# Kernel tuning notes

Measured on AMD Instinct MI355X. Metric: run time of the kernel, lower is better.

## Reference

```python
import jax, jax.numpy as jnp
import numpy as np

NEG_INF = jnp.float32(-1e30)


def setup_inputs() -> dict:
    key = jax.random.key(0)
    ks = jax.random.split(key, 7)
    B, Lx, Lm, d = 4, 256, 256, 256
    return {
        "x": jax.random.normal(ks[0], (B, Lx, d), dtype=jnp.float32),
        "memory": jax.random.normal(ks[1], (B, Lm, d), dtype=jnp.float32),
        "memory_mask": jax.random.randint(ks[2], (B, Lm), 0, 2, dtype=jnp.int32),
        "ws1_w": jax.random.normal(ks[3], (d, d), dtype=jnp.float32) * 0.05,
        "ws1_b": jax.random.normal(ks[4], (d,), dtype=jnp.float32) * 0.05,
        "ws2_w": jax.random.normal(ks[5], (d, d), dtype=jnp.float32) * 0.05,
        "wst_w": jax.random.normal(ks[6], (1, d), dtype=jnp.float32) * 0.05,
    }


def reference(x, memory, memory_mask, ws1_w, ws1_b, ws2_w, wst_w):
    # x: [B, Lx, d], memory: [B, Lm, d]; torch Linear: y = x @ W.T + b
    item1 = jnp.einsum('bxd,ed->bxe', x, ws1_w) + ws1_b          # [B, Lx, d]
    item2 = jnp.einsum('bmd,ed->bme', memory, ws2_w)             # [B, Lm, d]
    item = jnp.tanh(item1[:, :, None, :] + item2[:, None, :, :])  # [B, Lx, Lm, d]
    S = jnp.einsum('bxmd,d->bxm', item, wst_w[0])                # [B, Lx, Lm]
    # agg_2_h uses the UNMASKED scores, softmax over Lx after transpose
    agg_2_h = jnp.einsum('bmx,bxd->bmd', jax.nn.softmax(S.transpose(0, 2, 1), axis=-1), x)
    # mask applied to S before the main attention readout
    S = jnp.where(memory_mask[:, None, :] == 0, NEG_INF, S)      # [B, Lx, Lm]
    out = jnp.einsum('bxm,bmd->bxd', jax.nn.softmax(S, axis=-1), memory)
    return (out, S, agg_2_h)
```

## Files before the change

kernel.cpp:

```cpp
#include <hip/hip_runtime.h>

static constexpr int NB = 4;
static constexpr int L  = 256;
static constexpr int D  = 256;

__device__ __forceinline__ float fast_rcp(float x) {
#if __has_builtin(__builtin_amdgcn_rcpf)
    return __builtin_amdgcn_rcpf(x);
#else
    return 1.0f / x;
#endif
}

__device__ __forceinline__ float fast_exp(float x) {
#if __has_builtin(__builtin_amdgcn_exp2f)
    return __builtin_amdgcn_exp2f(x * 1.4426950408889634f);
#else
    return __expf(x);
#endif
}

__device__ __forceinline__ float tanh_fast(float y) {
#if __has_builtin(__builtin_amdgcn_exp2f)
    float e = __builtin_amdgcn_exp2f(y * 2.8853900817779268f);
#else
    float e = __expf(2.0f * y);
#endif
    return fmaf(-2.0f, fast_rcp(e + 1.0f), 1.0f);
}

__global__ __launch_bounds__(256) void linear_kernel(
    const float* __restrict__ x, const float* __restrict__ mem,
    const float* __restrict__ w1, const float* __restrict__ b1,
    const float* __restrict__ w2,
    float* __restrict__ i1, float* __restrict__ i2)
{
    const int bid = blockIdx.x;
    const int rb  = (bid >> 3) * 32;
    const int cb  = (bid & 7) * 32;
    const int which = rb >= 1024;
    const int rloc  = which ? rb - 1024 : rb;
    const float* src = which ? mem : x;
    const float* W   = which ? w2  : w1;
    float*       dst = which ? i2  : i1;

    constexpr int P4 = 65;
    __shared__ __align__(16) float4 xs4[32 * P4];
    __shared__ __align__(16) float4 ws4[32 * P4];

    const int t = threadIdx.x;
    const float4* src4 = reinterpret_cast<const float4*>(src) + rloc * 64;
    const float4* Wg4  = reinterpret_cast<const float4*>(W)   + cb   * 64;
#pragma unroll
    for (int k = 0; k < 8; ++k) {
        int idx = k * 256 + t;
        int r = idx >> 6, c = idx & 63;
        xs4[r * P4 + c] = src4[r * 64 + c];
        ws4[r * P4 + c] = Wg4[r * 64 + c];
    }
    __syncthreads();

    const int rr = t >> 4, cc = t & 15;
    const float4* a0p = xs4 + rr * P4;
    const float4* a1p = xs4 + (rr + 16) * P4;
    const float4* w0p = ws4 + cc * P4;
    const float4* w1p = ws4 + (cc + 16) * P4;
    float acc00 = 0.f, acc01 = 0.f, acc10 = 0.f, acc11 = 0.f;
#pragma unroll 4
    for (int d4 = 0; d4 < 64; ++d4) {
        float4 a0 = a0p[d4], a1 = a1p[d4];
        float4 w0 = w0p[d4], w1 = w1p[d4];
        acc00 = fmaf(a0.x, w0.x, acc00); acc00 = fmaf(a0.y, w0.y, acc00);
        acc00 = fmaf(a0.z, w0.z, acc00); acc00 = fmaf(a0.w, w0.w, acc00);
        acc01 = fmaf(a0.x, w1.x, acc01); acc01 = fmaf(a0.y, w1.y, acc01);
        acc01 = fmaf(a0.z, w1.z, acc01); acc01 = fmaf(a0.w, w1.w, acc01);
        acc10 = fmaf(a1.x, w0.x, acc10); acc10 = fmaf(a1.y, w0.y, acc10);
        acc10 = fmaf(a1.z, w0.z, acc10); acc10 = fmaf(a1.w, w0.w, acc10);
        acc11 = fmaf(a1.x, w1.x, acc11); acc11 = fmaf(a1.y, w1.y, acc11);
        acc11 = fmaf(a1.z, w1.z, acc11); acc11 = fmaf(a1.w, w1.w, acc11);
    }
    const float bias0 = which ? 0.f : b1[cb + cc];
    const float bias1 = which ? 0.f : b1[cb + cc + 16];
    dst[(rloc + rr)      * D + cb + cc]      = acc00 + bias0;
    dst[(rloc + rr)      * D + cb + cc + 16] = acc01 + bias1;
    dst[(rloc + rr + 16) * D + cb + cc]      = acc10 + bias0;
    dst[(rloc + rr + 16) * D + cb + cc + 16] = acc11 + bias1;
}

__global__ __launch_bounds__(256) void score_kernel(
    const float* __restrict__ i1, const float* __restrict__ i2,
    const float* __restrict__ wst, const int* __restrict__ mask,
    float* __restrict__ outS, float* __restrict__ ST)
{
    const int bid = blockIdx.x;
    const int b   = bid >> 8;
    const int xt  = ((bid >> 4) & 15) * 16;
    const int mt  = (bid & 15) * 16;
    const int t   = threadIdx.x;

    constexpr int PAD = 260;
    __shared__ __align__(16) float s1[16 * PAD];
    __shared__ __align__(16) float s2[16 * PAD];
    __shared__ float stile[16 * 17];

    const float4* i14 = reinterpret_cast<const float4*>(i1) + (b * L + xt) * (D / 4);
    const float4* i24 = reinterpret_cast<const float4*>(i2) + (b * L + mt) * (D / 4);
    float4* s14 = reinterpret_cast<float4*>(s1);
    float4* s24 = reinterpret_cast<float4*>(s2);
#pragma unroll
    for (int k = 0; k < 4; ++k) {
        int idx = k * 256 + t;
        int r = idx >> 6, c = idx & 63;
        s14[r * (PAD / 4) + c] = i14[r * (D / 4) + c];
        s24[r * (PAD / 4) + c] = i24[r * (D / 4) + c];
    }
    __syncthreads();

    const int xl = t >> 4, ml = t & 15;
    const float4* a4 = s14 + xl * (PAD / 4);
    const float4* b4 = s24 + ml * (PAD / 4);
    const float4* w4 = reinterpret_cast<const float4*>(wst);
    float acc = 0.0f;
#pragma unroll 4
    for (int d4 = 0; d4 < D / 4; ++d4) {
        float4 a  = a4[d4];
        float4 bb = b4[d4];
        float4 w  = w4[d4];
        acc = fmaf(tanh_fast(a.x + bb.x), w.x, acc);
        acc = fmaf(tanh_fast(a.y + bb.y), w.y, acc);
        acc = fmaf(tanh_fast(a.z + bb.z), w.z, acc);
        acc = fmaf(tanh_fast(a.w + bb.w), w.w, acc);
    }
    const int xi = xt + xl, mi = mt + ml;
    outS[((b * L + xi) << 8) + mi] = (mask[b * L + mi] == 0) ? -1e30f : acc;

    stile[ml * 17 + xl] = acc;
    __syncthreads();
    const int m2 = t >> 4, x2 = t & 15;
    ST[((b * L + mt + m2) << 8) + xt + x2] = stile[m2 * 17 + x2];
}

__global__ __launch_bounds__(256) void attn_kernel(
    const float* __restrict__ S1, const float* __restrict__ V1, float* __restrict__ out1,
    const float* __restrict__ S2, const float* __restrict__ V2, float* __restrict__ out2)
{
    int bid = blockIdx.x;
    const float* S; const float* V; float* out;
    if (bid < NB * L / 4) { S = S1; V = V1; out = out1; }
    else                  { S = S2; V = V2; out = out2; bid -= NB * L / 4; }

    const int row0 = bid * 4;
    const int b    = row0 >> 8;
    const int t    = threadIdx.x;
    const int w    = t >> 6, l = t & 63;

    __shared__ __align__(16) float p[4][L];
    __shared__ __align__(16) float4 part[4][4][64];

    {
        float4 sv = reinterpret_cast<const float4*>(S)[((row0 + w) << 6) + l];
        float m = fmaxf(fmaxf(sv.x, sv.y), fmaxf(sv.z, sv.w));
#pragma unroll
        for (int o = 32; o; o >>= 1) m = fmaxf(m, __shfl_xor(m, o));
        float e0 = fast_exp(sv.x - m), e1 = fast_exp(sv.y - m);
        float e2 = fast_exp(sv.z - m), e3 = fast_exp(sv.w - m);
        float s = (e0 + e1) + (e2 + e3);
#pragma unroll
        for (int o = 32; o; o >>= 1) s += __shfl_xor(s, o);
        float rs = fast_rcp(s);
        reinterpret_cast<float4*>(p[w])[l] = make_float4(e0 * rs, e1 * rs, e2 * rs, e3 * rs);
    }
    __syncthreads();

    const float4* V4 = reinterpret_cast<const float4*>(V) + (b * L) * (D / 4);
    float4 acc[4];
#pragma unroll
    for (int r = 0; r < 4; ++r) acc[r] = make_float4(0.f, 0.f, 0.f, 0.f);

#pragma unroll 4
    for (int k = 0; k < 64; ++k) {
        int mm = w * 64 + k;
        float4 v = V4[mm * (D / 4) + l];
#pragma unroll
        for (int r = 0; r < 4; ++r) {
            float pm = p[r][mm];
            acc[r].x = fmaf(pm, v.x, acc[r].x);
            acc[r].y = fmaf(pm, v.y, acc[r].y);
            acc[r].z = fmaf(pm, v.z, acc[r].z);
            acc[r].w = fmaf(pm, v.w, acc[r].w);
        }
    }
#pragma unroll
    for (int r = 0; r < 4; ++r) part[r][w][l] = acc[r];
    __syncthreads();

    {
        float4 r0 = part[w][0][l], r1 = part[w][1][l];
        float4 r2 = part[w][2][l], r3 = part[w][3][l];
        float4 o;
        o.x = (r0.x + r1.x) + (r2.x + r3.x);
        o.y = (r0.y + r1.y) + (r2.y + r3.y);
        o.z = (r0.z + r1.z) + (r2.z + r3.z);
        o.w = (r0.w + r1.w) + (r2.w + r3.w);
        reinterpret_cast<float4*>(out)[((row0 + w) << 6) + l] = o;
    }
}

extern "C" void kernel_launch(void* const* d_in, const int* in_sizes, int n_in,
                              void* d_out, int out_size, void* d_ws, size_t ws_size,
                              hipStream_t stream)
{
    const float* x    = (const float*)d_in[0];
    const float* mem  = (const float*)d_in[1];
    const int*   mask = (const int*)  d_in[2];
    const float* w1   = (const float*)d_in[3];
    const float* b1   = (const float*)d_in[4];
    const float* w2   = (const float*)d_in[5];
    const float* wst  = (const float*)d_in[6];

    float* out   = (float*)d_out;
    float* Smask = out + NB * L * L;
    float* agg   = Smask + NB * L * L;

    float* i1 = (float*)d_ws;
    float* i2 = i1 + NB * L * D;
    float* ST = i2 + NB * L * D;

    linear_kernel<<<512, 256, 0, stream>>>(x, mem, w1, b1, w2, i1, i2);
    score_kernel<<<NB * (L / 16) * (L / 16), 256, 0, stream>>>(i1, i2, wst, mask, Smask, ST);
    attn_kernel<<<2 * (NB * L / 4), 256, 0, stream>>>(Smask, mem, out, ST, x, agg);
}
```

Baseline: 39.88 us.

## Factor tanh exponent into per-side exp, 2x2 score tiles, 8-row attention blocks

The linear kernel now stores exp(2*item) instead of item, so the score kernel computes exp(2(a+b)) as a product of two precomputed exponentials. This removes the per-element transcendental from the Lx*Lm*d inner loop, leaving one multiply, one rcp and one fma. The score kernel also moves to 32x32 tiles with a 2x2 register block per thread, and the attention kernel handles 8 rows per block with float4 probability reads. Risks are overflow or inf in the exp product for large pre-activations, and fewer blocks (256 score, 256 attention), which lowers occupancy.

```diff
diff --git a/kernel.cpp b/kernel.cpp
--- a/kernel.cpp
+++ b/kernel.cpp
@@ -20,12 +20,15 @@
 #endif
 }
 
-__device__ __forceinline__ float tanh_fast(float y) {
+__device__ __forceinline__ float exp_2x(float x) {
 #if __has_builtin(__builtin_amdgcn_exp2f)
-    float e = __builtin_amdgcn_exp2f(y * 2.8853900817779268f);
+    return __builtin_amdgcn_exp2f(x * 2.8853900817779268f);
 #else
-    float e = __expf(2.0f * y);
+    return __expf(2.0f * x);
 #endif
+}
+
+__device__ __forceinline__ float tanh_from_e(float e) {
     return fmaf(-2.0f, fast_rcp(e + 1.0f), 1.0f);
 }
 
@@ -33,7 +36,7 @@
     const float* __restrict__ x, const float* __restrict__ mem,
     const float* __restrict__ w1, const float* __restrict__ b1,
     const float* __restrict__ w2,
-    float* __restrict__ i1, float* __restrict__ i2)
+    float* __restrict__ E1, float* __restrict__ E2)
 {
     const int bid = blockIdx.x;
     const int rb  = (bid >> 3) * 32;
@@ -42,7 +45,7 @@
     const int rloc  = which ? rb - 1024 : rb;
     const float* src = which ? mem : x;
     const float* W   = which ? w2  : w1;
-    float*       dst = which ? i2  : i1;
+    float*       dst = which ? E2  : E1;
 
     constexpr int P4 = 65;
     __shared__ __align__(16) float4 xs4[32 * P4];
@@ -81,63 +84,88 @@
     }
     const float bias0 = which ? 0.f : b1[cb + cc];
     const float bias1 = which ? 0.f : b1[cb + cc + 16];
-    dst[(rloc + rr)      * D + cb + cc]      = acc00 + bias0;
-    dst[(rloc + rr)      * D + cb + cc + 16] = acc01 + bias1;
-    dst[(rloc + rr + 16) * D + cb + cc]      = acc10 + bias0;
-    dst[(rloc + rr + 16) * D + cb + cc + 16] = acc11 + bias1;
+    dst[(rloc + rr)      * D + cb + cc]      = exp_2x(acc00 + bias0);
+    dst[(rloc + rr)      * D + cb + cc + 16] = exp_2x(acc01 + bias1);
+    dst[(rloc + rr + 16) * D + cb + cc]      = exp_2x(acc10 + bias0);
+    dst[(rloc + rr + 16) * D + cb + cc + 16] = exp_2x(acc11 + bias1);
 }
 
 __global__ __launch_bounds__(256) void score_kernel(
-    const float* __restrict__ i1, const float* __restrict__ i2,
+    const float* __restrict__ E1, const float* __restrict__ E2,
     const float* __restrict__ wst, const int* __restrict__ mask,
     float* __restrict__ outS, float* __restrict__ ST)
 {
     const int bid = blockIdx.x;
-    const int b   = bid >> 8;
-    const int xt  = ((bid >> 4) & 15) * 16;
-    const int mt  = (bid & 15) * 16;
+    const int b   = bid >> 6;
+    const int xt  = ((bid >> 3) & 7) * 32;
+    const int mt  = (bid & 7) * 32;
     const int t   = threadIdx.x;
 
-    constexpr int PAD = 260;
-    __shared__ __align__(16) float s1[16 * PAD];
-    __shared__ __align__(16) float s2[16 * PAD];
-    __shared__ float stile[16 * 17];
-
-    const float4* i14 = reinterpret_cast<const float4*>(i1) + (b * L + xt) * (D / 4);
-    const float4* i24 = reinterpret_cast<const float4*>(i2) + (b * L + mt) * (D / 4);
-    float4* s14 = reinterpret_cast<float4*>(s1);
-    float4* s24 = reinterpret_cast<float4*>(s2);
+    constexpr int P4 = 65;
+    __shared__ __align__(16) float4 s1[32 * P4];
+    __shared__ __align__(16) float4 s2[32 * P4];
+    __shared__ float stile[32 * 33];
+
+    const float4* e14 = reinterpret_cast<const float4*>(E1) + (b * L + xt) * 64;
+    const float4* e24 = reinterpret_cast<const float4*>(E2) + (b * L + mt) * 64;
+#pragma unroll
+    for (int k = 0; k < 8; ++k) {
+        int idx = k * 256 + t;
+        int r = idx >> 6, c = idx & 63;
+        s1[r * P4 + c] = e14[r * 64 + c];
+        s2[r * P4 + c] = e24[r * 64 + c];
+    }
+    __syncthreads();
+
+    const int rr = t >> 4, cc = t & 15;
+    const float4* a0p = s1 + rr * P4;
+    const float4* a1p = s1 + (rr + 16) * P4;
+    const float4* b0p = s2 + cc * P4;
+    const float4* b1p = s2 + (cc + 16) * P4;
+    const float4* w4  = reinterpret_cast<const float4*>(wst);
+    float acc00 = 0.f, acc01 = 0.f, acc10 = 0.f, acc11 = 0.f;
+#pragma unroll 4
+    for (int d4 = 0; d4 < 64; ++d4) {
+        float4 a0 = a0p[d4], a1 = a1p[d4];
+        float4 b0 = b0p[d4], b1 = b1p[d4];
+        float4 w  = w4[d4];
+        acc00 = fmaf(tanh_from_e(a0.x * b0.x), w.x, acc00);
+        acc00 = fmaf(tanh_from_e(a0.y * b0.y), w.y, acc00);
+        acc00 = fmaf(tanh_from_e(a0.z * b0.z), w.z, acc00);
+        acc00 = fmaf(tanh_from_e(a0.w * b0.w), w.w, acc00);
+        acc01 = fmaf(tanh_from_e(a0.x * b1.x), w.x, acc01);
+        acc01 = fmaf(tanh_from_e(a0.y * b1.y), w.y, acc01);
+        acc01 = fmaf(tanh_from_e(a0.z * b1.z), w.z, acc01);
+        acc01 = fmaf(tanh_from_e(a0.w * b1.w), w.w, acc01);
+        acc10 = fmaf(tanh_from_e(a1.x * b0.x), w.x, acc10);
+        acc10 = fmaf(tanh_from_e(a1.y * b0.y), w.y, acc10);
+        acc10 = fmaf(tanh_from_e(a1.z * b0.z), w.z, acc10);
+        acc10 = fmaf(tanh_from_e(a1.w * b0.w), w.w, acc10);
+        acc11 = fmaf(tanh_from_e(a1.x * b1.x), w.x, acc11);
+        acc11 = fmaf(tanh_from_e(a1.y * b1.y), w.y, acc11);
+        acc11 = fmaf(tanh_from_e(a1.z * b1.z), w.z, acc11);
+        acc11 = fmaf(tanh_from_e(a1.w * b1.w), w.w, acc11);
+    }
+
+    const int m0 = mt + cc, m1 = mt + cc + 16;
+    const int x0 = xt + rr, x1 = xt + rr + 16;
+    const bool k0 = (mask[b * L + m0] == 0), k1 = (mask[b * L + m1] == 0);
+    outS[((b * L + x0) << 8) + m0] = k0 ? -1e30f : acc00;
+    outS[((b * L + x0) << 8) + m1] = k1 ? -1e30f : acc01;
+    outS[((b * L + x1) << 8) + m0] = k0 ? -1e30f : acc10;
+    outS[((b * L + x1) << 8) + m1] = k1 ? -1e30f : acc11;
+
+    stile[cc        * 33 + rr]      = acc00;
+    stile[(cc + 16) * 33 + rr]      = acc01;
+    stile[cc        * 33 + rr + 16] = acc10;
+    stile[(cc + 16) * 33 + rr + 16] = acc11;
+    __syncthreads();
 #pragma unroll
     for (int k = 0; k < 4; ++k) {
         int idx = k * 256 + t;
-        int r = idx >> 6, c = idx & 63;
-        s14[r * (PAD / 4) + c] = i14[r * (D / 4) + c];
-        s24[r * (PAD / 4) + c] = i24[r * (D / 4) + c];
-    }
-    __syncthreads();
-
-    const int xl = t >> 4, ml = t & 15;
-    const float4* a4 = s14 + xl * (PAD / 4);
-    const float4* b4 = s24 + ml * (PAD / 4);
-    const float4* w4 = reinterpret_cast<const float4*>(wst);
-    float acc = 0.0f;
-#pragma unroll 4
-    for (int d4 = 0; d4 < D / 4; ++d4) {
-        float4 a  = a4[d4];
-        float4 bb = b4[d4];
-        float4 w  = w4[d4];
-        acc = fmaf(tanh_fast(a.x + bb.x), w.x, acc);
-        acc = fmaf(tanh_fast(a.y + bb.y), w.y, acc);
-        acc = fmaf(tanh_fast(a.z + bb.z), w.z, acc);
-        acc = fmaf(tanh_fast(a.w + bb.w), w.w, acc);
-    }
-    const int xi = xt + xl, mi = mt + ml;
-    outS[((b * L + xi) << 8) + mi] = (mask[b * L + mi] == 0) ? -1e30f : acc;
-
-    stile[ml * 17 + xl] = acc;
-    __syncthreads();
-    const int m2 = t >> 4, x2 = t & 15;
-    ST[((b * L + mt + m2) << 8) + xt + x2] = stile[m2 * 17 + x2];
+        int mr = idx >> 5, xc = idx & 31;
+        ST[((b * L + mt + mr) << 8) + xt + xc] = stile[mr * 33 + xc];
+    }
 }
 
 __global__ __launch_bounds__(256) void attn_kernel(
@@ -146,19 +174,20 @@
 {
     int bid = blockIdx.x;
     const float* S; const float* V; float* out;
-    if (bid < NB * L / 4) { S = S1; V = V1; out = out1; }
-    else                  { S = S2; V = V2; out = out2; bid -= NB * L / 4; }
-
-    const int row0 = bid * 4;
+    if (bid < NB * L / 8) { S = S1; V = V1; out = out1; }
+    else                  { S = S2; V = V2; out = out2; bid -= NB * L / 8; }
+
+    const int row0 = bid * 8;
     const int b    = row0 >> 8;
     const int t    = threadIdx.x;
     const int w    = t >> 6, l = t & 63;
 
-    __shared__ __align__(16) float p[4][L];
-    __shared__ __align__(16) float4 part[4][4][64];
-
-    {
-        float4 sv = reinterpret_cast<const float4*>(S)[((row0 + w) << 6) + l];
+    __shared__ __align__(16) float p[8][L];
+    __shared__ __align__(16) float4 part[8][4][64];
+
+#pragma unroll
+    for (int rr = w; rr < 8; rr += 4) {
+        float4 sv = reinterpret_cast<const float4*>(S)[((row0 + rr) << 6) + l];
         float m = fmaxf(fmaxf(sv.x, sv.y), fmaxf(sv.z, sv.w));
 #pragma unroll
         for (int o = 32; o; o >>= 1) m = fmaxf(m, __shfl_xor(m, o));
@@ -168,41 +197,49 @@
 #pragma unroll
         for (int o = 32; o; o >>= 1) s += __shfl_xor(s, o);
         float rs = fast_rcp(s);
-        reinterpret_cast<float4*>(p[w])[l] = make_float4(e0 * rs, e1 * rs, e2 * rs, e3 * rs);
-    }
-    __syncthreads();
-
-    const float4* V4 = reinterpret_cast<const float4*>(V) + (b * L) * (D / 4);
-    float4 acc[4];
-#pragma unroll
-    for (int r = 0; r < 4; ++r) acc[r] = make_float4(0.f, 0.f, 0.f, 0.f);
-
-#pragma unroll 4
-    for (int k = 0; k < 64; ++k) {
-        int mm = w * 64 + k;
-        float4 v = V4[mm * (D / 4) + l];
-#pragma unroll
-        for (int r = 0; r < 4; ++r) {
-            float pm = p[r][mm];
-            acc[r].x = fmaf(pm, v.x, acc[r].x);
-            acc[r].y = fmaf(pm, v.y, acc[r].y);
-            acc[r].z = fmaf(pm, v.z, acc[r].z);
-            acc[r].w = fmaf(pm, v.w, acc[r].w);
+        reinterpret_cast<float4*>(p[rr])[l] = make_float4(e0 * rs, e1 * rs, e2 * rs, e3 * rs);
+    }
+    __syncthreads();
+
+    const float4* V4 = reinterpret_cast<const float4*>(V) + (b * L) * 64;
+    float4 acc[8];
+#pragma unroll
+    for (int r = 0; r < 8; ++r) acc[r] = make_float4(0.f, 0.f, 0.f, 0.f);
+
+#pragma unroll 2
+    for (int k4 = 0; k4 < 16; ++k4) {
+        const int m0 = w * 64 + k4 * 4;
+        float4 v0 = V4[(m0 + 0) * 64 + l];
+        float4 v1 = V4[(m0 + 1) * 64 + l];
+        float4 v2 = V4[(m0 + 2) * 64 + l];
+        float4 v3 = V4[(m0 + 3) * 64 + l];
+#pragma unroll
+        for (int r = 0; r < 8; ++r) {
+            float4 pr = *reinterpret_cast<const float4*>(&p[r][m0]);
+            acc[r].x = fmaf(pr.x, v0.x, acc[r].x); acc[r].y = fmaf(pr.x, v0.y, acc[r].y);
+            acc[r].z = fmaf(pr.x, v0.z, acc[r].z); acc[r].w = fmaf(pr.x, v0.w, acc[r].w);
+            acc[r].x = fmaf(pr.y, v1.x, acc[r].x); acc[r].y = fmaf(pr.y, v1.y, acc[r].y);
+            acc[r].z = fmaf(pr.y, v1.z, acc[r].z); acc[r].w = fmaf(pr.y, v1.w, acc[r].w);
+            acc[r].x = fmaf(pr.z, v2.x, acc[r].x); acc[r].y = fmaf(pr.z, v2.y, acc[r].y);
+            acc[r].z = fmaf(pr.z, v2.z, acc[r].z); acc[r].w = fmaf(pr.z, v2.w, acc[r].w);
+            acc[r].x = fmaf(pr.w, v3.x, acc[r].x); acc[r].y = fmaf(pr.w, v3.y, acc[r].y);
+            acc[r].z = fmaf(pr.w, v3.z, acc[r].z); acc[r].w = fmaf(pr.w, v3.w, acc[r].w);
         }
     }
 #pragma unroll
-    for (int r = 0; r < 4; ++r) part[r][w][l] = acc[r];
-    __syncthreads();
-
-    {
-        float4 r0 = part[w][0][l], r1 = part[w][1][l];
-        float4 r2 = part[w][2][l], r3 = part[w][3][l];
+    for (int r = 0; r < 8; ++r) part[r][w][l] = acc[r];
+    __syncthreads();
+
+#pragma unroll
+    for (int rr = w; rr < 8; rr += 4) {
+        float4 r0 = part[rr][0][l], r1 = part[rr][1][l];
+        float4 r2 = part[rr][2][l], r3 = part[rr][3][l];
         float4 o;
         o.x = (r0.x + r1.x) + (r2.x + r3.x);
         o.y = (r0.y + r1.y) + (r2.y + r3.y);
         o.z = (r0.z + r1.z) + (r2.z + r3.z);
         o.w = (r0.w + r1.w) + (r2.w + r3.w);
-        reinterpret_cast<float4*>(out)[((row0 + w) << 6) + l] = o;
+        reinterpret_cast<float4*>(out)[((row0 + rr) << 6) + l] = o;
     }
 }
 
@@ -222,11 +259,11 @@
     float* Smask = out + NB * L * L;
     float* agg   = Smask + NB * L * L;
 
-    float* i1 = (float*)d_ws;
-    float* i2 = i1 + NB * L * D;
-    float* ST = i2 + NB * L * D;
-
-    linear_kernel<<<512, 256, 0, stream>>>(x, mem, w1, b1, w2, i1, i2);
-    score_kernel<<<NB * (L / 16) * (L / 16), 256, 0, stream>>>(i1, i2, wst, mask, Smask, ST);
-    attn_kernel<<<2 * (NB * L / 4), 256, 0, stream>>>(Smask, mem, out, ST, x, agg);
-}
+    float* E1 = (float*)d_ws;
+    float* E2 = E1 + NB * L * D;
+    float* ST = E2 + NB * L * D;
+
+    linear_kernel<<<512, 256, 0, stream>>>(x, mem, w1, b1, w2, E1, E2);
+    score_kernel<<<NB * (L / 32) * (L / 32), 256, 0, stream>>>(E1, E2, wst, mask, Smask, ST);
+    attn_kernel<<<2 * (NB * L / 8), 256, 0, stream>>>(Smask, mem, out, ST, x, agg);
+}
```

After: 38.84 us. 1.03x faster.
